# Optimization experiments

Measured on AMD Instinct MI355X. Metric: run time of the kernel, lower is better.

The kernel has to match this reference:

```python
import jax, jax.numpy as jnp
import numpy as np
import math

N_HEAD = 16

def _c(a):
    # stack real/imag -> complex64
    return jax.lax.complex(a[..., 0], a[..., 1])

def _rope_phasor(T, D, dtype=jnp.float32):
    inv_freq = 1.0 / (10000.0 ** (jnp.arange(D, dtype=dtype) / D))
    t = jnp.arange(T, dtype=dtype)
    freqs = jnp.outer(t, inv_freq)  # [T, D]
    return jax.lax.complex(jnp.cos(freqs), jnp.sin(freqs))

def setup_inputs() -> dict:
    key = jax.random.key(0)
    ks = jax.random.split(key, 9)
    B, T, C = 2, 1024, 1024
    s = 0.02
    return {
        "x":  jax.random.normal(ks[0], (B, T, C, 2), jnp.float32),
        "wq": jax.random.normal(ks[1], (C, C, 2), jnp.float32) * s,
        "bq": jax.random.normal(ks[2], (C, 2), jnp.float32) * s,
        "wk": jax.random.normal(ks[3], (C, C, 2), jnp.float32) * s,
        "bk": jax.random.normal(ks[4], (C, 2), jnp.float32) * s,
        "wv": jax.random.normal(ks[5], (C, C, 2), jnp.float32) * s,
        "bv": jax.random.normal(ks[6], (C, 2), jnp.float32) * s,
        "wo": jax.random.normal(ks[7], (C, C, 2), jnp.float32) * s,
        "bo": jax.random.normal(ks[8], (C, 2), jnp.float32) * s,
    }

def reference(x, wq, bq, wk, bk, wv, bv, wo, bo):
    B, T, C, _ = x.shape
    H = N_HEAD
    D = C // H
    xc = _c(x)
    # complex linear projections: y = x @ W^T + b
    q = xc @ _c(wq).T + _c(bq)
    k = xc @ _c(wk).T + _c(bk)
    v = xc @ _c(wv).T + _c(bv)
    # [B, T, C] -> [B, H, T, D]
    q = q.reshape(B, T, H, D).transpose(0, 2, 1, 3)
    k = k.reshape(B, T, H, D).transpose(0, 2, 1, 3)
    v = v.reshape(B, T, H, D).transpose(0, 2, 1, 3)
    # complex RoPE phasor multiply
    ph = _rope_phasor(T, D)[None, None]  # [1,1,T,D]
    q = q * ph
    k = k * ph
    # complex QK^H, scaled
    score = jnp.einsum('bhtd,bhsd->bhts', q, jnp.conj(k)) / math.sqrt(D)
    # softmax over magnitude, then real-valued complex weights
    attn = jax.nn.softmax(jnp.abs(score), axis=-1)
    attn_c = jax.lax.complex(attn, jnp.zeros_like(attn))
    out = jnp.einsum('bhts,bhsd->bhtd', attn_c, v)
    out = out.transpose(0, 2, 1, 3).reshape(B, T, C)
    out = out @ _c(wo).T + _c(bo)
    # return real/imag stacked for a real-valued harness
    return jnp.stack([out.real, out.imag], axis=-1)
```

## Files before the change

### kernel.cpp

```cpp
#include <hip/hip_runtime.h>
#include <math.h>

#define T_SEQ  1024
#define C_DIM  1024
#define NH_    16
#define H_DIM  64
#define SCL    (0.125f * 1.4426950408889634f)

typedef __bf16 bf16;
typedef __bf16 bf16x4 __attribute__((ext_vector_type(4)));
typedef __bf16 bf16x8 __attribute__((ext_vector_type(8)));
typedef float  f32x4  __attribute__((ext_vector_type(4)));

template<bool B> struct BC { static constexpr bool value = B; };

#define MFMA16(a, b, c) __builtin_amdgcn_mfma_f32_16x16x32_bf16(a, b, c, 0, 0, 0)

#define GLOAD_LDS16(g, l) __builtin_amdgcn_global_load_lds( \
    (const __attribute__((address_space(1))) void*)(g),     \
    (__attribute__((address_space(3))) void*)(l), 16, 0, 0)

__device__ __forceinline__ bf16x8 neg8(bf16x8 x) {
    union { bf16x8 v; unsigned int u[4]; } t;
    t.v = x;
    t.u[0] ^= 0x80008000u; t.u[1] ^= 0x80008000u;
    t.u[2] ^= 0x80008000u; t.u[3] ^= 0x80008000u;
    return t.v;
}

__device__ __forceinline__ bf16x8 frag_sw(const bf16* plane, int row, int chunk) {
    int c = chunk ^ (row & 7);
    return *(const bf16x8*)&plane[row * 64 + c * 8];
}
__device__ __forceinline__ bf16x8 frag_sw4(const bf16* plane, int row, int chunk) {
    int c = chunk ^ (row & 3);
    return *(const bf16x8*)&plane[row * 32 + c * 8];
}
__device__ __forceinline__ bf16x8 frag_sw4b(const bf16* plane, int row, int chunk) {
    int c = chunk ^ ((row >> 1) & 3);
    return *(const bf16x8*)&plane[row * 32 + c * 8];
}

__global__ __launch_bounds__(256)
void split_all(const float* __restrict__ x,  const float* __restrict__ wq,
               const float* __restrict__ wk, const float* __restrict__ wv,
               const float* __restrict__ wo,
               bf16* Xr, bf16* Xi, bf16* Wqr, bf16* Wqi, bf16* Wkr, bf16* Wki,
               bf16* Wvr, bf16* Wvi, bf16* Wor, bf16* Woi,
               float* __restrict__ rope)
{
    int z = blockIdx.y;
    if (z == 5) {
        if (blockIdx.x >= 256) return;
        int idx = blockIdx.x * 256 + threadIdx.x;
        int tp = idx >> 6, d = idx & 63;
        float invf = exp2f((float)d * -0.2076205059304601f);
        float fr = (float)tp * invf;
        float sn, cs; sincosf(fr, &sn, &cs);
        *(float2*)&rope[(size_t)idx * 2] = make_float2(cs, sn);
        return;
    }
    if (z > 0 && blockIdx.x >= 512) return;
    const float* in; bf16 *pr, *pi;
    if      (z == 0) { in = x;  pr = Xr;  pi = Xi;  }
    else if (z == 1) { in = wq; pr = Wqr; pi = Wqi; }
    else if (z == 2) { in = wk; pr = Wkr; pi = Wki; }
    else if (z == 3) { in = wv; pr = Wvr; pi = Wvi; }
    else             { in = wo; pr = Wor; pi = Woi; }
    int idx = (blockIdx.x * 256 + threadIdx.x) * 8;
    bf16x8 r, im;
#pragma unroll
    for (int j = 0; j < 4; j++) {
        float4 v = *(const float4*)(in + (size_t)idx * 2 + j * 4);
        r[2*j]   = (bf16)v.x; im[2*j]   = (bf16)v.y;
        r[2*j+1] = (bf16)v.z; im[2*j+1] = (bf16)v.w;
    }
    *(bf16x8*)(pr + idx) = r;
    *(bf16x8*)(pi + idx) = im;
}

__global__ __launch_bounds__(512, 2)
void qkv_gemm(const bf16* __restrict__ Xr, const bf16* __restrict__ Xi,
              const bf16* __restrict__ Wqr, const bf16* __restrict__ Wqi,
              const bf16* __restrict__ Wkr, const bf16* __restrict__ Wki,
              const bf16* __restrict__ Wvr, const bf16* __restrict__ Wvi,
              const float* __restrict__ bq, const float* __restrict__ bk,
              const float* __restrict__ bv, const float* __restrict__ rope,
              bf16* Qr, bf16* Qi, bf16* Kr, bf16* Ki, bf16* Vr, bf16* Vi)
{
    __shared__ __attribute__((aligned(16))) bf16 smem[61440];
    const int t = threadIdx.x, lane = t & 63, wave = t >> 6;
    const int wm = (wave >> 1) * 32, wn = (wave & 1) * 32;
    const int lm = lane & 15, quad = lane >> 4;
    const int lr4 = lane >> 2, sc4q = ((lane & 3) ^ ((lane >> 3) & 3)) * 8;
    const int h = blockIdx.x, m0 = blockIdx.y * 128, n0 = h * 64;

    auto stage1 = [&](bf16* bb_, int j, int k0) {
        int c = wave + 8 * j;
        const bf16* src; bf16* dst;
        if (c < 8)       {                 src = Xr  + (size_t)(m0 + c * 16 + lr4) * C_DIM + k0 + sc4q; dst = bb_ + c * 512; }
        else if (c < 16) { int u = c - 8;  src = Xi  + (size_t)(m0 + u * 16 + lr4) * C_DIM + k0 + sc4q; dst = bb_ + 4096  + u * 512; }
        else if (c < 20) { int u = c - 16; src = Wqr + (size_t)(n0 + u * 16 + lr4) * C_DIM + k0 + sc4q; dst = bb_ + 8192  + u * 512; }
        else if (c < 24) { int u = c - 20; src = Wqi + (size_t)(n0 + u * 16 + lr4) * C_DIM + k0 + sc4q; dst = bb_ + 10240 + u * 512; }
        else if (c < 28) { int u = c - 24; src = Wkr + (size_t)(n0 + u * 16 + lr4) * C_DIM + k0 + sc4q; dst = bb_ + 12288 + u * 512; }
        else if (c < 32) { int u = c - 28; src = Wki + (size_t)(n0 + u * 16 + lr4) * C_DIM + k0 + sc4q; dst = bb_ + 14336 + u * 512; }
        else if (c < 36) { int u = c - 32; src = Wvr + (size_t)(n0 + u * 16 + lr4) * C_DIM + k0 + sc4q; dst = bb_ + 16384 + u * 512; }
        else             { int u = c - 36; src = Wvi + (size_t)(n0 + u * 16 + lr4) * C_DIM + k0 + sc4q; dst = bb_ + 18432 + u * 512; }
        GLOAD_LDS16(src, dst);
    };

    f32x4 accr[3][2][2], acci[3][2][2];
#pragma unroll
    for (int p = 0; p < 3; p++)
#pragma unroll
        for (int i = 0; i < 2; i++)
#pragma unroll
            for (int j = 0; j < 2; j++) { accr[p][i][j] = (f32x4)0.f; acci[p][i][j] = (f32x4)0.f; }

    auto step = [&](auto DOSTAGE, auto DRAIN, int bufsel, int sbsel, int k2) {
        const bf16* buf = smem + bufsel * 20480;
        bf16* sb = smem + sbsel * 20480;
        if constexpr (DRAIN.value)
            asm volatile("s_waitcnt vmcnt(0)\n\ts_barrier" ::: "memory");
        else
            asm volatile("s_waitcnt vmcnt(5)\n\ts_barrier" ::: "memory");

        bf16x8 ar[2], ai_[2];
        bf16x8 bqr[2], bqi[2], bkr[2], bki[2], bvr[2], bvi[2], bn_[2];
#pragma unroll
        for (int i = 0; i < 2; i++) {
            ar[i]  = frag_sw4b(buf,        wm + i * 16 + lm, quad);
            ai_[i] = frag_sw4b(buf + 4096, wm + i * 16 + lm, quad);
        }
#pragma unroll
        for (int j = 0; j < 2; j++) {
            bqr[j] = frag_sw4b(buf + 8192,  wn + j * 16 + lm, quad);
            bqi[j] = frag_sw4b(buf + 10240, wn + j * 16 + lm, quad);
        }
#pragma unroll
        for (int j = 0; j < 2; j++) {
            bkr[j] = frag_sw4b(buf + 12288, wn + j * 16 + lm, quad);
            bki[j] = frag_sw4b(buf + 14336, wn + j * 16 + lm, quad);
        }
        if constexpr (DOSTAGE.value) { stage1(sb, 0, k2); stage1(sb, 1, k2); }
        asm volatile("s_waitcnt lgkmcnt(4)" ::: "memory");
        __builtin_amdgcn_sched_barrier(0);
        __builtin_amdgcn_s_setprio(1);
#pragma unroll
        for (int j = 0; j < 2; j++) bn_[j] = neg8(bqi[j]);
#pragma unroll
        for (int i = 0; i < 2; i++)
#pragma unroll
            for (int j = 0; j < 2; j++) {
                accr[0][i][j] = MFMA16(ar[i],  bqr[j], accr[0][i][j]);
                accr[0][i][j] = MFMA16(ai_[i], bn_[j], accr[0][i][j]);
                acci[0][i][j] = MFMA16(ar[i],  bqi[j], acci[0][i][j]);
                acci[0][i][j] = MFMA16(ai_[i], bqr[j], acci[0][i][j]);
            }
        __builtin_amdgcn_s_setprio(0);
#pragma unroll
        for (int j = 0; j < 2; j++) {
            bvr[j] = frag_sw4b(buf + 16384, wn + j * 16 + lm, quad);
            bvi[j] = frag_sw4b(buf + 18432, wn + j * 16 + lm, quad);
        }
        if constexpr (DOSTAGE.value) { stage1(sb, 2, k2); stage1(sb, 3, k2); }
        asm volatile("s_waitcnt lgkmcnt(4)" ::: "memory");
        __builtin_amdgcn_sched_barrier(0);
        __builtin_amdgcn_s_setprio(1);
#pragma unroll
        for (int j = 0; j < 2; j++) bn_[j] = neg8(bki[j]);
#pragma unroll
        for (int i = 0; i < 2; i++)
#pragma unroll
            for (int j = 0; j < 2; j++) {
                accr[1][i][j] = MFMA16(ar[i],  bkr[j], accr[1][i][j]);
                accr[1][i][j] = MFMA16(ai_[i], bn_[j], accr[1][i][j]);
                acci[1][i][j] = MFMA16(ar[i],  bki[j], acci[1][i][j]);
                acci[1][i][j] = MFMA16(ai_[i], bkr[j], acci[1][i][j]);
            }
        __builtin_amdgcn_s_setprio(0);
        if constexpr (DOSTAGE.value) { stage1(sb, 4, k2); }
        asm volatile("s_waitcnt lgkmcnt(0)" ::: "memory");
        __builtin_amdgcn_sched_barrier(0);
        __builtin_amdgcn_s_setprio(1);
#pragma unroll
        for (int j = 0; j < 2; j++) bn_[j] = neg8(bvi[j]);
#pragma unroll
        for (int i = 0; i < 2; i++)
#pragma unroll
            for (int j = 0; j < 2; j++) {
                accr[2][i][j] = MFMA16(ar[i],  bvr[j], accr[2][i][j]);
                accr[2][i][j] = MFMA16(ai_[i], bn_[j], accr[2][i][j]);
                acci[2][i][j] = MFMA16(ar[i],  bvi[j], acci[2][i][j]);
                acci[2][i][j] = MFMA16(ai_[i], bvr[j], acci[2][i][j]);
            }
        __builtin_amdgcn_s_setprio(0);
    };

#pragma unroll
    for (int j = 0; j < 5; j++) stage1(smem,         j, 0);
#pragma unroll
    for (int j = 0; j < 5; j++) stage1(smem + 20480, j, 32);

    for (int base = 0; base < 30; base += 3) {
        step(BC<true>{}, BC<false>{}, 0, 2, (base + 2) * 32);
        step(BC<true>{}, BC<false>{}, 1, 0, (base + 3) * 32);
        step(BC<true>{}, BC<false>{}, 2, 1, (base + 4) * 32);
    }
    step(BC<false>{}, BC<false>{}, 0, 0, 0);
    step(BC<false>{}, BC<true >{}, 1, 0, 0);

    const int bb = m0 >> 10, tbase = m0 & (T_SEQ - 1);

#pragma unroll
    for (int p = 0; p < 2; p++) {
        const float* bias = p ? bk : bq;
#pragma unroll
        for (int i = 0; i < 2; i++)
#pragma unroll
            for (int j = 0; j < 2; j++) {
                int d = wn + j * 16 + lm;
                float2 bvv = *(const float2*)&bias[2 * (n0 + d)];
#pragma unroll
                for (int r = 0; r < 4; r++) {
                    int tpos = tbase + wm + i * 16 + quad * 4 + r;
                    float2 ph = *(const float2*)&rope[((size_t)tpos * H_DIM + d) * 2];
                    float yr = accr[p][i][j][r] + bvv.x;
                    float yi = acci[p][i][j][r] + bvv.y;
                    accr[p][i][j][r] = yr * ph.x - yi * ph.y;
                    acci[p][i][j][r] = yr * ph.y + yi * ph.x;
                }
            }
        bf16* dr = (p ? Kr : Qr) + ((size_t)(bb * NH_ + h) * T_SEQ + tbase) * H_DIM;
        bf16* di = (p ? Ki : Qi) + ((size_t)(bb * NH_ + h) * T_SEQ + tbase) * H_DIM;
#pragma unroll
        for (int pass = 0; pass < 2; pass++) {
            __syncthreads();
#pragma unroll
            for (int i = 0; i < 2; i++)
#pragma unroll
                for (int j = 0; j < 2; j++)
#pragma unroll
                    for (int r = 0; r < 4; r++)
                        smem[(wm + i * 16 + quad * 4 + r) * 72 + wn + j * 16 + lm] =
                            (bf16)(pass ? acci[p][i][j][r] : accr[p][i][j][r]);
            __syncthreads();
            bf16* dst = pass ? di : dr;
#pragma unroll
            for (int pp = 0; pp < 2; pp++) {
                int ch = t + 512 * pp;
                int row = ch >> 3, o = (ch & 7) * 8;
                *(bf16x8*)&dst[row * H_DIM + o] = *(const bf16x8*)&smem[row * 72 + o];
            }
        }
    }

    {
#pragma unroll
        for (int pass = 0; pass < 2; pass++) {
            __syncthreads();
#pragma unroll
            for (int i = 0; i < 2; i++)
#pragma unroll
                for (int j = 0; j < 2; j++) {
                    int d = wn + j * 16 + lm;
                    float2 bvv = *(const float2*)&bv[2 * (n0 + d)];
                    float bb2 = pass ? bvv.y : bvv.x;
                    bf16x4 pk;
#pragma unroll
                    for (int r = 0; r < 4; r++)
                        pk[r] = (bf16)((pass ? acci[2][i][j][r] : accr[2][i][j][r]) + bb2);
                    *(bf16x4*)&smem[d * 136 + wm + i * 16 + quad * 4] = pk;
                }
            __syncthreads();
            bf16* dst = (pass ? Vi : Vr) + ((size_t)(bb * NH_ + h) * H_DIM) * T_SEQ + tbase;
#pragma unroll
            for (int pp = 0; pp < 2; pp++) {
                int ch = t + 512 * pp;
                int row = ch >> 4, o = (ch & 15) * 8;
                *(bf16x8*)&dst[(size_t)row * T_SEQ + o] = *(const bf16x8*)&smem[row * 136 + o];
            }
        }
    }
}

__global__ __launch_bounds__(256, 4)
void out_gemm(const bf16* __restrict__ Ar, const bf16* __restrict__ Ai,
              const bf16* __restrict__ Br, const bf16* __restrict__ Bi,
              const float* __restrict__ bias, float* __restrict__ Y)
{
    __shared__ __attribute__((aligned(16))) bf16 sm[16384];
    const int t = threadIdx.x, lane = t & 63, wave = t >> 6;
    const int lm = lane & 15, quad = lane >> 4;
    const int s_lr = lane >> 3, s_c = (lane & 7) ^ s_lr;
    const int wm = (wave >> 1) * 32, wn = (wave & 1) * 32;
    const int m0 = blockIdx.y * 64, n0 = blockIdx.x * 64;

    f32x4 accr[2][2], acci[2][2];
#pragma unroll
    for (int i = 0; i < 2; i++)
#pragma unroll
        for (int j = 0; j < 2; j++) { accr[i][j] = (f32x4)0.f; acci[i][j] = (f32x4)0.f; }

    for (int k0 = 0; k0 < C_DIM; k0 += 64) {
#pragma unroll
        for (int j = 0; j < 8; j++) {
            int c = wave + 4 * j;
            const bf16* src; bf16* dst;
            if (c < 8)       {             src = Ar + (size_t)(m0 + c * 8 + s_lr) * C_DIM + k0 + s_c * 8; dst = sm + c * 512; }
            else if (c < 16) { int u = c - 8;  src = Ai + (size_t)(m0 + u * 8 + s_lr) * C_DIM + k0 + s_c * 8; dst = sm + 4096 + u * 512; }
            else if (c < 24) { int u = c - 16; src = Br + (size_t)(n0 + u * 8 + s_lr) * C_DIM + k0 + s_c * 8; dst = sm + 8192 + u * 512; }
            else             { int u = c - 24; src = Bi + (size_t)(n0 + u * 8 + s_lr) * C_DIM + k0 + s_c * 8; dst = sm + 12288 + u * 512; }
            GLOAD_LDS16(src, dst);
        }
        __syncthreads();
#pragma unroll
        for (int kh = 0; kh < 2; kh++) {
            bf16x8 ar[2], ai_[2], br_[2], bi_[2], bn_[2];
#pragma unroll
            for (int i = 0; i < 2; i++) {
                ar[i]  = frag_sw(sm,        wm + i * 16 + lm, kh * 4 + quad);
                ai_[i] = frag_sw(sm + 4096, wm + i * 16 + lm, kh * 4 + quad);
            }
#pragma unroll
            for (int j = 0; j < 2; j++) {
                br_[j] = frag_sw(sm + 8192,  wn + j * 16 + lm, kh * 4 + quad);
                bi_[j] = frag_sw(sm + 12288, wn + j * 16 + lm, kh * 4 + quad);
                bn_[j] = neg8(bi_[j]);
            }
#pragma unroll
            for (int i = 0; i < 2; i++)
#pragma unroll
                for (int j = 0; j < 2; j++) {
                    accr[i][j] = MFMA16(ar[i],  br_[j], accr[i][j]);
                    accr[i][j] = MFMA16(ai_[i], bn_[j], accr[i][j]);
                    acci[i][j] = MFMA16(ar[i],  bi_[j], acci[i][j]);
                    acci[i][j] = MFMA16(ai_[i], br_[j], acci[i][j]);
                }
        }
        __syncthreads();
    }
#pragma unroll
    for (int i = 0; i < 2; i++)
#pragma unroll
        for (int j = 0; j < 2; j++) {
            int n = n0 + wn + j * 16 + lm;
            float2 bvv = *(const float2*)&bias[2 * n];
#pragma unroll
            for (int r = 0; r < 4; r++) {
                int m = m0 + wm + i * 16 + quad * 4 + r;
                *(float2*)&Y[((size_t)m * C_DIM + n) * 2] =
                    make_float2(accr[i][j][r] + bvv.x, acci[i][j][r] + bvv.y);
            }
        }
}

__global__ __launch_bounds__(512, 4)
void attn_mfma(const bf16* __restrict__ Qpr, const bf16* __restrict__ Qpi,
               const bf16* __restrict__ Kpr, const bf16* __restrict__ Kpi,
               const bf16* __restrict__ Vtr, const bf16* __restrict__ Vti,
               bf16* __restrict__ ABr, bf16* __restrict__ ABi)
{
    __shared__ __attribute__((aligned(16))) bf16 smem[32768];
    const int t = threadIdx.x, lane = t & 63, w = t >> 6;
    const int qg = w & 3, sh = w >> 2;
    const int lm = lane & 15, quad = lane >> 4;
    const int h = blockIdx.x;
    const int q0 = blockIdx.y * 64;
    const int b = blockIdx.z;
    const size_t hb = (size_t)(b * NH_ + h) * T_SEQ * H_DIM;
    const int s_lr = lane >> 3, s_c = (lane & 7) ^ s_lr;
    const int lr4 = lane >> 2, sc4a = ((lane & 3) ^ (lr4 & 3)) * 8;

    {
        const bf16* gq = (sh ? Qpi : Qpr) + hb + (size_t)q0 * H_DIM;
        bf16* lq = smem + 16384 + sh * 4096;
#pragma unroll
        for (int j = 0; j < 2; j++) {
            int cc = qg * 2 + j;
            GLOAD_LDS16(gq + (cc * 8 + s_lr) * H_DIM + s_c * 8, lq + cc * 512);
        }
    }
    __syncthreads();

    bf16x8 qfr[2], qfi[2], nqfr[2];
#pragma unroll
    for (int kh = 0; kh < 2; kh++) {
        qfr[kh]  = frag_sw(smem + 16384, qg * 16 + lm, kh * 4 + quad);
        qfi[kh]  = frag_sw(smem + 20480, qg * 16 + lm, kh * 4 + quad);
        nqfr[kh] = neg8(qfr[kh]);
    }

#pragma unroll
    for (int pre = 0; pre < 1; pre++) {
        const int S = sh * 512;
        bf16* bd = smem + sh * 8192;
        if (qg < 2) {
            const bf16* g = (qg ? Kpi : Kpr) + hb + (size_t)S * H_DIM;
            bf16* d = bd + (qg ? 2048 : 0);
#pragma unroll
            for (int cc = 0; cc < 4; cc++)
                GLOAD_LDS16(g + (cc * 8 + s_lr) * H_DIM + s_c * 8, d + cc * 512);
        } else {
            const bf16* g = (qg == 2 ? Vtr : Vti) + hb + S;
            bf16* d = bd + (qg == 2 ? 4096 : 6144);
#pragma unroll
            for (int cc = 0; cc < 4; cc++)
                GLOAD_LDS16(g + (size_t)(cc * 16 + lr4) * T_SEQ + sc4a, d + cc * 512);
        }
    }

    f32x4 Or[4], Oi[4];
#pragma unroll
    for (int nt = 0; nt < 4; nt++) { Or[nt] = (f32x4)0.f; Oi[nt] = (f32x4)0.f; }
    float lsum = 0.f;
    const int idxA = (((2 * quad) & 3) * 16 + lm) * 4;
    const int idxB = idxA + 64;
    const bool hisel = quad >= 2;

    for (int it = 0; it < 16; it++) {
        __syncthreads();
        if (it < 15) {
            const int S = (it + 1) * 32 + sh * 512;
            bf16* bd = smem + ((it + 1) & 1) * 16384 + sh * 8192;
            if (qg < 2) {
                const bf16* g = (qg ? Kpi : Kpr) + hb + (size_t)S * H_DIM;
                bf16* d = bd + (qg ? 2048 : 0);
#pragma unroll
                for (int cc = 0; cc < 4; cc++)
                    GLOAD_LDS16(g + (cc * 8 + s_lr) * H_DIM + s_c * 8, d + cc * 512);
            } else {
                const bf16* g = (qg == 2 ? Vtr : Vti) + hb + S;
                bf16* d = bd + (qg == 2 ? 4096 : 6144);
#pragma unroll
                for (int cc = 0; cc < 4; cc++)
                    GLOAD_LDS16(g + (size_t)(cc * 16 + lr4) * T_SEQ + sc4a, d + cc * 512);
            }
        }
        const bf16* buf = smem + (it & 1) * 16384 + sh * 8192;

        union { unsigned int u[2]; bf16 b[4]; } pk[2];
        float lsA = 0.f, lsB = 0.f;
#pragma unroll
        for (int ct = 0; ct < 2; ct++) {
            f32x4 sre = (f32x4)0.f, sim = (f32x4)0.f;
            __builtin_amdgcn_s_setprio(1);
#pragma unroll
            for (int kh = 0; kh < 2; kh++) {
                bf16x8 kr = frag_sw(buf,        ct * 16 + lm, kh * 4 + quad);
                bf16x8 ki = frag_sw(buf + 2048, ct * 16 + lm, kh * 4 + quad);
                sre = MFMA16(kr, qfr[kh],  sre);
                sre = MFMA16(ki, qfi[kh],  sre);
                sim = MFMA16(kr, qfi[kh],  sim);
                sim = MFMA16(ki, nqfr[kh], sim);
            }
            __builtin_amdgcn_s_setprio(0);
#pragma unroll
            for (int r = 0; r < 4; r++) {
                float mag2 = fmaf(sre[r], sre[r], sim[r] * sim[r]);
                float p = __builtin_amdgcn_exp2f(__builtin_amdgcn_sqrtf(mag2) * SCL);
                if (ct) lsB += p; else lsA += p;
                pk[ct].b[r] = (bf16)p;
            }
        }
        lsum += lsA + lsB;

        union { unsigned int u[4]; bf16x8 v; } pf;
        {
            int a0 = __builtin_amdgcn_ds_bpermute(idxA, (int)pk[0].u[0]);
            int a1 = __builtin_amdgcn_ds_bpermute(idxA, (int)pk[1].u[0]);
            int b0 = __builtin_amdgcn_ds_bpermute(idxA, (int)pk[0].u[1]);
            int b1 = __builtin_amdgcn_ds_bpermute(idxA, (int)pk[1].u[1]);
            int c0 = __builtin_amdgcn_ds_bpermute(idxB, (int)pk[0].u[0]);
            int c1 = __builtin_amdgcn_ds_bpermute(idxB, (int)pk[1].u[0]);
            int d0 = __builtin_amdgcn_ds_bpermute(idxB, (int)pk[0].u[1]);
            int d1 = __builtin_amdgcn_ds_bpermute(idxB, (int)pk[1].u[1]);
            pf.u[0] = (unsigned int)(hisel ? a1 : a0);
            pf.u[1] = (unsigned int)(hisel ? b1 : b0);
            pf.u[2] = (unsigned int)(hisel ? c1 : c0);
            pf.u[3] = (unsigned int)(hisel ? d1 : d0);
        }

        __builtin_amdgcn_s_setprio(1);
#pragma unroll
        for (int nt = 0; nt < 4; nt++) {
            Or[nt] = MFMA16(pf.v, frag_sw4(buf + 4096, nt * 16 + lm, quad), Or[nt]);
            Oi[nt] = MFMA16(pf.v, frag_sw4(buf + 6144, nt * 16 + lm, quad), Oi[nt]);
        }
        __builtin_amdgcn_s_setprio(0);
    }

    lsum += __shfl_xor(lsum, 16);
    lsum += __shfl_xor(lsum, 32);

    __syncthreads();
    float* Of  = (float*)smem;
    float* lsc = Of + 128 * 66;
    if (sh == 1) {
#pragma unroll
        for (int nt = 0; nt < 4; nt++)
#pragma unroll
            for (int r = 0; r < 4; r++) {
                Of[((qg * 2 + 0) * 16 + quad * 4 + r) * 66 + nt * 16 + lm] = Or[nt][r];
                Of[((qg * 2 + 1) * 16 + quad * 4 + r) * 66 + nt * 16 + lm] = Oi[nt][r];
            }
        if (quad == 0) lsc[qg * 16 + lm] = lsum;
    }
    __syncthreads();
    if (sh == 0) {
        float ltot = lsum + lsc[qg * 16 + lm];
        float lv = 1.f / ltot;
        float linv[4];
#pragma unroll
        for (int r = 0; r < 4; r++)
            linv[r] = __shfl(lv, (quad << 4) + quad * 4 + r, 64);
        size_t mbase = (size_t)(b * T_SEQ + q0 + qg * 16 + quad * 4) * C_DIM;
        int colb = h * H_DIM + lm;
#pragma unroll
        for (int nt = 0; nt < 4; nt++)
#pragma unroll
            for (int r = 0; r < 4; r++) {
                float orv = Or[nt][r] + Of[((qg * 2 + 0) * 16 + quad * 4 + r) * 66 + nt * 16 + lm];
                float oiv = Oi[nt][r] + Of[((qg * 2 + 1) * 16 + quad * 4 + r) * 66 + nt * 16 + lm];
                size_t o = mbase + (size_t)r * C_DIM + colb + nt * 16;
                ABr[o] = (bf16)(orv * linv[r]);
                ABi[o] = (bf16)(oiv * linv[r]);
            }
    }
}

extern "C" void kernel_launch(void* const* d_in, const int* in_sizes, int n_in,
                              void* d_out, int out_size, void* d_ws, size_t ws_size,
                              hipStream_t stream) {
    const float* x  = (const float*)d_in[0];
    const float* wq = (const float*)d_in[1];
    const float* bq = (const float*)d_in[2];
    const float* wk = (const float*)d_in[3];
    const float* bk = (const float*)d_in[4];
    const float* wv = (const float*)d_in[5];
    const float* bv = (const float*)d_in[6];
    const float* wo = (const float*)d_in[7];
    const float* bo = (const float*)d_in[8];

    float* rope = (float*)d_ws;
    bf16* w = (bf16*)(rope + 131072);
    const size_t MSZ = (size_t)2048 * 1024;
    const size_t WSZ = (size_t)1024 * 1024;
    const size_t PSZ = (size_t)2 * NH_ * T_SEQ * H_DIM;

    bf16 *Xr = w, *Xi = Xr + MSZ;
    bf16 *Wqr = Xi + MSZ,  *Wqi = Wqr + WSZ;
    bf16 *Wkr = Wqi + WSZ, *Wki = Wkr + WSZ;
    bf16 *Wvr = Wki + WSZ, *Wvi = Wvr + WSZ;
    bf16 *Wor = Wvi + WSZ, *Woi = Wor + WSZ;
    bf16 *Qr = Woi + WSZ, *Qi = Qr + PSZ;
    bf16 *Kr = Qi + PSZ,  *Ki = Kr + PSZ;
    bf16 *Vr = Ki + PSZ,  *Vi = Vr + PSZ;
    bf16 *ABr = Vi + PSZ, *ABi = ABr + MSZ;

    split_all<<<dim3(1024, 6), 256, 0, stream>>>(x, wq, wk, wv, wo,
        Xr, Xi, Wqr, Wqi, Wkr, Wki, Wvr, Wvi, Wor, Woi, rope);

    qkv_gemm<<<dim3(16, 16), 512, 0, stream>>>(
        Xr, Xi, Wqr, Wqi, Wkr, Wki, Wvr, Wvi, bq, bk, bv, rope,
        Qr, Qi, Kr, Ki, Vr, Vi);

    attn_mfma<<<dim3(16, 16, 2), 512, 0, stream>>>(
        Qr, Qi, Kr, Ki, Vr, Vi, ABr, ABi);

    out_gemm<<<dim3(16, 32), 256, 0, stream>>>(ABr, ABi, Wor, Woi, bo, (float*)d_out);
}
```

Before: 207.8 us.

## Triple-buffer out_gemm LDS with async global-to-LDS prefetch pipeline

Rewrites the output projection GEMM main loop into a three-stage software pipeline with K=32 slices, issuing direct global-to-LDS loads for future slices while computing the current one. Explicit vmcnt waits and a single barrier per step replace the two syncthreads per K=64 tile, and MFMA sections are given raised wave priority. The LDS swizzle layout changes to match the 32-wide slices. Shared memory use grows, so occupancy is lowered to 3 blocks per CU.

```diff
diff --git a/kernel.cpp b/kernel.cpp
--- a/kernel.cpp
+++ b/kernel.cpp
@@ -284,62 +284,87 @@
     }
 }
 
-__global__ __launch_bounds__(256, 4)
+__global__ __launch_bounds__(256, 3)
 void out_gemm(const bf16* __restrict__ Ar, const bf16* __restrict__ Ai,
               const bf16* __restrict__ Br, const bf16* __restrict__ Bi,
               const float* __restrict__ bias, float* __restrict__ Y)
 {
-    __shared__ __attribute__((aligned(16))) bf16 sm[16384];
+    __shared__ __attribute__((aligned(16))) bf16 sm[24576];
     const int t = threadIdx.x, lane = t & 63, wave = t >> 6;
     const int lm = lane & 15, quad = lane >> 4;
-    const int s_lr = lane >> 3, s_c = (lane & 7) ^ s_lr;
+    const int lr4 = lane >> 2, sc4q = ((lane & 3) ^ ((lane >> 3) & 3)) * 8;
     const int wm = (wave >> 1) * 32, wn = (wave & 1) * 32;
     const int m0 = blockIdx.y * 64, n0 = blockIdx.x * 64;
 
+    auto stage1 = [&](bf16* bb_, int j, int k0) {
+        int c = wave + 4 * j;
+        const bf16* src; bf16* dst;
+        if (c < 4)       {                 src = Ar + (size_t)(m0 + c * 16 + lr4) * C_DIM + k0 + sc4q; dst = bb_ + c * 512; }
+        else if (c < 8)  { int u = c - 4;  src = Ai + (size_t)(m0 + u * 16 + lr4) * C_DIM + k0 + sc4q; dst = bb_ + 2048 + u * 512; }
+        else if (c < 12) { int u = c - 8;  src = Br + (size_t)(n0 + u * 16 + lr4) * C_DIM + k0 + sc4q; dst = bb_ + 4096 + u * 512; }
+        else             { int u = c - 12; src = Bi + (size_t)(n0 + u * 16 + lr4) * C_DIM + k0 + sc4q; dst = bb_ + 6144 + u * 512; }
+        GLOAD_LDS16(src, dst);
+    };
+
     f32x4 accr[2][2], acci[2][2];
 #pragma unroll
     for (int i = 0; i < 2; i++)
 #pragma unroll
         for (int j = 0; j < 2; j++) { accr[i][j] = (f32x4)0.f; acci[i][j] = (f32x4)0.f; }
 
-    for (int k0 = 0; k0 < C_DIM; k0 += 64) {
-#pragma unroll
-        for (int j = 0; j < 8; j++) {
-            int c = wave + 4 * j;
-            const bf16* src; bf16* dst;
-            if (c < 8)       {             src = Ar + (size_t)(m0 + c * 8 + s_lr) * C_DIM + k0 + s_c * 8; dst = sm + c * 512; }
-            else if (c < 16) { int u = c - 8;  src = Ai + (size_t)(m0 + u * 8 + s_lr) * C_DIM + k0 + s_c * 8; dst = sm + 4096 + u * 512; }
-            else if (c < 24) { int u = c - 16; src = Br + (size_t)(n0 + u * 8 + s_lr) * C_DIM + k0 + s_c * 8; dst = sm + 8192 + u * 512; }
-            else             { int u = c - 24; src = Bi + (size_t)(n0 + u * 8 + s_lr) * C_DIM + k0 + s_c * 8; dst = sm + 12288 + u * 512; }
-            GLOAD_LDS16(src, dst);
-        }
-        __syncthreads();
-#pragma unroll
-        for (int kh = 0; kh < 2; kh++) {
-            bf16x8 ar[2], ai_[2], br_[2], bi_[2], bn_[2];
-#pragma unroll
-            for (int i = 0; i < 2; i++) {
-                ar[i]  = frag_sw(sm,        wm + i * 16 + lm, kh * 4 + quad);
-                ai_[i] = frag_sw(sm + 4096, wm + i * 16 + lm, kh * 4 + quad);
-            }
+    auto step = [&](auto DOSTAGE, auto DRAIN, int bufsel, int sbsel, int k2) {
+        const bf16* buf = sm + bufsel * 8192;
+        bf16* sb = sm + sbsel * 8192;
+        if constexpr (DRAIN.value)
+            asm volatile("s_waitcnt vmcnt(0)\n\ts_barrier" ::: "memory");
+        else
+            asm volatile("s_waitcnt vmcnt(4)\n\ts_barrier" ::: "memory");
+
+        bf16x8 ar[2], ai_[2], br_[2], bi_[2], bn_[2];
+#pragma unroll
+        for (int i = 0; i < 2; i++) {
+            ar[i]  = frag_sw4b(buf,        wm + i * 16 + lm, quad);
+            ai_[i] = frag_sw4b(buf + 2048, wm + i * 16 + lm, quad);
+        }
+#pragma unroll
+        for (int j = 0; j < 2; j++) {
+            br_[j] = frag_sw4b(buf + 4096, wn + j * 16 + lm, quad);
+            bi_[j] = frag_sw4b(buf + 6144, wn + j * 16 + lm, quad);
+        }
+        if constexpr (DOSTAGE.value) {
+            stage1(sb, 0, k2); stage1(sb, 1, k2);
+            stage1(sb, 2, k2); stage1(sb, 3, k2);
+        }
+        asm volatile("s_waitcnt lgkmcnt(0)" ::: "memory");
+        __builtin_amdgcn_sched_barrier(0);
+        __builtin_amdgcn_s_setprio(1);
+#pragma unroll
+        for (int j = 0; j < 2; j++) bn_[j] = neg8(bi_[j]);
+#pragma unroll
+        for (int i = 0; i < 2; i++)
 #pragma unroll
             for (int j = 0; j < 2; j++) {
-                br_[j] = frag_sw(sm + 8192,  wn + j * 16 + lm, kh * 4 + quad);
-                bi_[j] = frag_sw(sm + 12288, wn + j * 16 + lm, kh * 4 + quad);
-                bn_[j] = neg8(bi_[j]);
-            }
-#pragma unroll
-            for (int i = 0; i < 2; i++)
-#pragma unroll
-                for (int j = 0; j < 2; j++) {
-                    accr[i][j] = MFMA16(ar[i],  br_[j], accr[i][j]);
-                    accr[i][j] = MFMA16(ai_[i], bn_[j], accr[i][j]);
-                    acci[i][j] = MFMA16(ar[i],  bi_[j], acci[i][j]);
-                    acci[i][j] = MFMA16(ai_[i], br_[j], acci[i][j]);
-                }
-        }
-        __syncthreads();
-    }
+                accr[i][j] = MFMA16(ar[i],  br_[j], accr[i][j]);
+                accr[i][j] = MFMA16(ai_[i], bn_[j], accr[i][j]);
+                acci[i][j] = MFMA16(ar[i],  bi_[j], acci[i][j]);
+                acci[i][j] = MFMA16(ai_[i], br_[j], acci[i][j]);
+            }
+        __builtin_amdgcn_s_setprio(0);
+    };
+
+#pragma unroll
+    for (int j = 0; j < 4; j++) stage1(sm,        j, 0);
+#pragma unroll
+    for (int j = 0; j < 4; j++) stage1(sm + 8192, j, 32);
+
+    for (int base = 0; base < 30; base += 3) {
+        step(BC<true>{}, BC<false>{}, 0, 2, (base + 2) * 32);
+        step(BC<true>{}, BC<false>{}, 1, 0, (base + 3) * 32);
+        step(BC<true>{}, BC<false>{}, 2, 1, (base + 4) * 32);
+    }
+    step(BC<false>{}, BC<false>{}, 0, 0, 0);
+    step(BC<false>{}, BC<true >{}, 1, 0, 0);
+
 #pragma unroll
     for (int i = 0; i < 2; i++)
 #pragma unroll
```

Result: no change. 206.5 us, median of 2 (-0.6%).
